# Kernel tuning notes

Measured on AMD Instinct MI355X. Metric: run time of the kernel, lower is better.

The kernel has to match this reference:

```python
import jax, jax.numpy as jnp
import numpy as np

# Irreps config: input/output = 32x0e + 16x1o (dim 80), H=4 heads -> head = 8x0e + 4x1o (dim 20)
M0, M1 = 32, 16      # input muls for 0e / 1o
m0, m1 = 8, 4        # per-head muls
H = 4
HEAD_DIM = m0 + 3 * m1   # 20
WNUM = H * (M0 * m0 + M1 * m0 + M0 * m1 + M1 * m1)  # 2304 per-edge TP weights
NB, HID = 16, 64
SQRT3 = np.float32(np.sqrt(3.0))
EPS = 1e-8


def radial_mlp(x, W1, b1, W2, b2):
    return jax.nn.silu(x @ W1 + b1) @ W2 + b2


def tp_edge(ss, vv, sh0, sh1, w):
    """FullyConnectedTensorProduct (32x0e+16x1o) x (1x0e+1x1o) -> H*(8x0e+4x1o) with per-edge weights w [E, WNUM].
    Paths: 0e*0e->0e, 1o*1o->0e (CG dot/sqrt3), 0e*1o->1o, 1o*0e->1o; path norm 1/sqrt(fan_in)."""
    E = ss.shape[0]
    per = M0 * m0 + M1 * m0 + M0 * m1 + M1 * m1  # 576
    w = w.reshape(E, H, per)
    o = 0
    Wss = w[..., o:o + M0 * m0].reshape(E, H, M0, m0); o += M0 * m0
    Wvv = w[..., o:o + M1 * m0].reshape(E, H, M1, m0); o += M1 * m0
    Wsv = w[..., o:o + M0 * m1].reshape(E, H, M0, m1); o += M0 * m1
    Wvs = w[..., o:o + M1 * m1].reshape(E, H, M1, m1)
    fan = np.float32(np.sqrt(M0 + M1))  # fan_in = 48 for both output irreps
    vv_dot = jnp.einsum('eui,ei->eu', vv, sh1) / SQRT3
    out0 = (jnp.einsum('eu,ehuw->ehw', ss * sh0[:, None], Wss)
            + jnp.einsum('eu,ehuw->ehw', vv_dot, Wvv)) / fan          # [E,H,m0]
    out1 = (jnp.einsum('eu,ehuw->ehw', ss, Wsv)[..., None] * sh1[:, None, None, :]
            + jnp.einsum('eui,ehuw->ehwi', vv * sh0[:, None, None], Wvs)) / fan  # [E,H,m1,3]
    return out0, out1


def setup_inputs() -> dict:
    key = jax.random.key(0)
    ks = jax.random.split(key, 24)
    N, E = 2000, 32000
    g = lambda k, s, sc=1.0: jax.random.normal(k, s, jnp.float32) * sc
    inp = {}
    inp['node_features'] = g(ks[0], (N, M0 + 3 * M1))
    inp['edge_index'] = jax.random.randint(ks[1], (2, E), 0, N)
    inp['edge_sh'] = g(ks[2], (E, 4))
    inp['edge_radial_emb'] = jax.random.uniform(ks[3], (E, NB), jnp.float32)
    # query e3nn Linear (per-head blocks)
    inp['Wq0'] = g(ks[4], (H, M0, m0))
    inp['Wq1'] = g(ks[5], (H, M1, m1))
    # radial MLPs for key / value TP weights
    inp['Wk1'] = g(ks[6], (NB, HID), 1 / np.sqrt(NB)); inp['bk1'] = jnp.zeros((HID,), jnp.float32)
    inp['Wk2'] = g(ks[7], (HID, WNUM), 1 / np.sqrt(HID)); inp['bk2'] = jnp.zeros((WNUM,), jnp.float32)
    inp['Wv1'] = g(ks[8], (NB, HID), 1 / np.sqrt(NB)); inp['bv1'] = jnp.zeros((HID,), jnp.float32)
    inp['Wv2'] = g(ks[9], (HID, WNUM), 1 / np.sqrt(HID)); inp['bv2'] = jnp.zeros((WNUM,), jnp.float32)
    # single-head dot-product TP -> 0e (shared weights)
    inp['Wd0'] = g(ks[10], (m0, m0))
    inp['Wd1'] = g(ks[11], (m1, m1))
    # output projection Linear (all heads mixed per irrep)
    inp['Wo0'] = g(ks[12], (H * m0, M0))
    inp['Wo1'] = g(ks[13], (H * m1, M1))
    # FFN: out irreps -> (2*M0)x0e + M1x1o -> out irreps
    inp['Wf1_0'] = g(ks[14], (M0, 2 * M0))
    inp['Wf1_1'] = g(ks[15], (M1, M1))
    inp['Wf2_0'] = g(ks[16], (2 * M0, M0))
    inp['Wf2_1'] = g(ks[17], (M1, M1))
    return inp


def reference(node_features, edge_index, edge_sh, edge_radial_emb,
              Wq0, Wq1, Wk1, bk1, Wk2, bk2, Wv1, bv1, Wv2, bv2,
              Wd0, Wd1, Wo0, Wo1, Wf1_0, Wf1_1, Wf2_0, Wf2_1):
    N = node_features.shape[0]
    s = node_features[:, :M0]                       # [N, M0] scalars
    v = node_features[:, M0:].reshape(N, M1, 3)     # [N, M1, 3] vectors
    src, dst = edge_index[0], edge_index[1]

    # query Linear (e3nn: per-irrep channel mix, norm 1/sqrt(fan_in))
    q0 = jnp.einsum('nu,huw->nhw', s, Wq0) / np.sqrt(M0)
    q1 = jnp.einsum('nui,huw->nhwi', v, Wq1) / np.sqrt(M1)

    sh0, sh1 = edge_sh[:, 0], edge_sh[:, 1:4]
    ss, vv = s[src], v[src]                         # gather per edge

    wk = radial_mlp(edge_radial_emb, Wk1, bk1, Wk2, bk2)
    wv = radial_mlp(edge_radial_emb, Wv1, bv1, Wv2, bv2)
    k0, k1 = tp_edge(ss, vv, sh0, sh1, wk)
    v0, v1 = tp_edge(ss, vv, sh0, sh1, wv)

    # per-head equivariant dot product -> 0e logits
    qd0, qd1 = q0[dst], q1[dst]
    fan_d = np.float32(np.sqrt(m0 * m0 + m1 * m1))
    logits = (jnp.einsum('ehu,uv,ehv->eh', qd0, Wd0, k0)
              + jnp.einsum('ehui,uv,ehvi->eh', qd1, Wd1, k1) / SQRT3) / fan_d
    logits = logits / np.sqrt(HEAD_DIM)             # self.scale
    logits = jnp.clip(logits, -10.0, 10.0)

    # scatter softmax over edges sharing a destination node
    seg_max = jax.ops.segment_max(logits, dst, num_segments=N)
    seg_max = jnp.maximum(seg_max, -10.0)           # handle empty segments
    ex = jnp.exp(logits - seg_max[dst])
    denom = jax.ops.segment_sum(ex, dst, num_segments=N)
    alpha = ex / (denom[dst] + 1e-12)               # [E, H]

    agg0 = jax.ops.segment_sum(alpha[..., None] * v0, dst, num_segments=N)        # [N,H,m0]
    agg1 = jax.ops.segment_sum(alpha[..., None, None] * v1, dst, num_segments=N)  # [N,H,m1,3]

    # output projection Linear over concatenated heads
    o0 = agg0.reshape(N, H * m0) @ Wo0 / np.sqrt(H * m0)
    o1 = jnp.einsum('nui,uw->nwi', agg1.reshape(N, H * m1, 3), Wo1) / np.sqrt(H * m1)

    # residual (input irreps == output irreps -> identity skip)
    x0 = s + o0
    x1 = v + o1

    # FFN with SafeNormActivation
    f0 = x0 @ Wf1_0 / np.sqrt(M0)                               # [N, 2*M0]
    f1 = jnp.einsum('nui,uw->nwi', x1, Wf1_1) / np.sqrt(M1)     # [N, M1, 3]
    a0 = jax.nn.silu(f0)
    norms = jnp.linalg.norm(f1, axis=-1, keepdims=True)
    safe = jnp.maximum(norms, EPS)
    a1 = jnp.where(norms < EPS, 0.0, (f1 / safe) * jax.nn.silu(norms))
    g0 = a0 @ Wf2_0 / np.sqrt(2 * M0)
    g1 = jnp.einsum('nui,uw->nwi', a1, Wf2_1) / np.sqrt(M1)

    out0 = x0 + g0
    out1 = x1 + g1
    return jnp.concatenate([out0, out1.reshape(N, M1 * 3)], axis=-1)
```

## Files before the change

### kernel.cpp

```cpp
#include <hip/hip_runtime.h>

typedef unsigned int uint;
typedef unsigned short ushort;
typedef __attribute__((ext_vector_type(8))) short bf16x8;
typedef __attribute__((ext_vector_type(4))) float f32x4;

#define N_NODES 2000
#define N_EDGES 32000
#define WNUM 2304

constexpr size_t OFF_AGG0 = 0;
constexpr size_t OFF_AGG1 = 64000;
constexpr size_t OFF_DEN  = 160000;
constexpr size_t OFF_CNT  = 168000;
constexpr size_t OFF_FLAG = 170000;
constexpr size_t OFF_W2T  = 170004;
constexpr size_t OFF_QT0  = 317460;
constexpr size_t OFF_QT1  = 381460;
constexpr size_t OFF_EORD = 477460;

__device__ __forceinline__ float b2f(ushort u){ union{uint i; float f;}x; x.i=((uint)u)<<16; return x.f; }
__device__ __forceinline__ float lo16(uint w){ union{uint u; float f;}x; x.u=w<<16; return x.f; }
__device__ __forceinline__ float hi16(uint w){ union{uint u; float f;}x; x.u=w&0xFFFF0000u; return x.f; }
__device__ __forceinline__ ushort f2b(float f){
  union{float f; uint u;}x; x.f=f;
  uint r = (x.u + 0x7FFFu + ((x.u>>16)&1u)) >> 16;
  return (ushort)r;
}
__device__ __forceinline__ float siluf(float x){ return x / (1.f + __expf(-x)); }

template<bool F32>
__device__ __forceinline__ float ldf(const void* p, int i){
  if (F32) return ((const float*)p)[i];
  return b2f(((const ushort*)p)[i]);
}
__device__ __forceinline__ float ldfr(const void* p, int i, bool f32){
  return f32 ? ((const float*)p)[i] : b2f(((const ushort*)p)[i]);
}

template<bool F32>
__device__ void prep_body(
    const void* __restrict__ nf, const int* __restrict__ eidx,
    const void* __restrict__ Wk2, const void* __restrict__ Wv2,
    const void* __restrict__ Wq0, const void* __restrict__ Wq1,
    const void* __restrict__ Wd0, const void* __restrict__ Wd1,
    ushort* __restrict__ W2T, float* __restrict__ qt0, float* __restrict__ qt1,
    int* __restrict__ cnt){
  const int t = threadIdx.x;
  const int bid = blockIdx.x;

  if (bid < 72){
    __shared__ ushort tile[64][66];
    const int mat = bid / 36, jt = bid - mat*36;
    const void* W = mat ? Wv2 : Wk2;
    const int j0 = jt*64;
    const int jo = t & 63, cb = t >> 6;
    #pragma unroll
    for (int k=0; k<16; ++k){
      const int c = cb + k*4;
      tile[c][jo] = F32 ? f2b(((const float*)W)[(size_t)c*WNUM + j0 + jo])
                        : ((const ushort*)W)[(size_t)c*WNUM + j0 + jo];
    }
    __syncthreads();
    const int jl = t >> 2, c0 = (t & 3)*16;
    ushort* dst = W2T + (size_t)mat*147456 + (size_t)(j0+jl)*64 + c0;
    #pragma unroll
    for (int k=0; k<16; ++k) dst[k] = tile[c0+k][jl];
  } else if (bid < 104){
    __shared__ float nfL[64][80];
    __shared__ float wq0L[1024], wq1L[256], wd0L[64], wd1L[16];
    const int nb = bid - 72, n0 = nb*64;
    for (int idx=t; idx<64*80; idx+=256){
      const int nn = n0 + idx/80;
      nfL[idx/80][idx%80] = (nn < N_NODES) ? ldf<F32>(nf, nn*80 + idx%80) : 0.f;
    }
    for (int idx=t; idx<1024; idx+=256) wq0L[idx] = ldf<F32>(Wq0, idx);
    if (t < 256) wq1L[t] = ldf<F32>(Wq1, t);
    if (t < 64)  wd0L[t] = ldf<F32>(Wd0, t);
    if (t < 16)  wd1L[t] = ldf<F32>(Wd1, t);
    __syncthreads();
    const int nl = t >> 2, h = t & 3;
    const int nn = n0 + nl;
    if (nn < N_NODES){
      const float* S = &nfL[nl][0];
      float q0[8];
      #pragma unroll
      for (int w=0; w<8; ++w){
        float a = 0.f;
        #pragma unroll
        for (int u=0; u<32; ++u) a += S[u]*wq0L[h*256 + u*8 + w];
        q0[w] = a * 0.17677669529663687f;
      }
      #pragma unroll
      for (int vv=0; vv<8; ++vv){
        float a = 0.f;
        #pragma unroll
        for (int u=0; u<8; ++u) a += q0[u]*wd0L[u*8+vv];
        qt0[nn*32 + h*8 + vv] = a;
      }
      float q1[12];
      #pragma unroll
      for (int w=0; w<4; ++w)
        #pragma unroll
        for (int i=0; i<3; ++i){
          float a = 0.f;
          #pragma unroll
          for (int u=0; u<16; ++u) a += S[32+u*3+i]*wq1L[h*64 + u*4 + w];
          q1[w*3+i] = a * 0.25f;
        }
      #pragma unroll
      for (int vv=0; vv<4; ++vv)
        #pragma unroll
        for (int i=0; i<3; ++i){
          float a = 0.f;
          #pragma unroll
          for (int u=0; u<4; ++u) a += q1[u*3+i]*wd1L[u*4+vv];
          qt1[nn*48 + h*12 + vv*3 + i] = a;
        }
    }
  } else {
    const int e = (bid-104)*256 + t;
    if (e < N_EDGES) atomicAdd(cnt + eidx[N_EDGES + e], 1);
  }
}

__global__ __launch_bounds__(256) void prep_kernel(
    const void* nf, const int* eidx,
    const void* Wk2, const void* Wv2,
    const void* Wq0, const void* Wq1,
    const void* Wd0, const void* Wd1,
    ushort* W2T, float* qt0, float* qt1,
    int* cnt, int* flag){
  __shared__ int s_cnt;
  const int t = threadIdx.x;
  if (t == 0) s_cnt = 0;
  __syncthreads();
  {
    uint u = ((const ushort*)nf)[t*2];
    uint ex = (u >> 7) & 0xFFu;
    if (ex >= 0xA0u) atomicAdd(&s_cnt, 1);
  }
  __syncthreads();
  const bool F32 = (s_cnt >= 20);
  if (blockIdx.x == 0 && t == 0) *flag = F32 ? 1 : 0;
  if (F32) prep_body<true >(nf, eidx, Wk2, Wv2, Wq0, Wq1, Wd0, Wd1, W2T, qt0, qt1, cnt);
  else     prep_body<false>(nf, eidx, Wk2, Wv2, Wq0, Wq1, Wd0, Wd1, W2T, qt0, qt1, cnt);
}

__global__ __launch_bounds__(256) void scan_kernel(int* __restrict__ cnt){
  __shared__ int ls[256];
  const int t = threadIdx.x;
  const int base = t*8;
  int v[8]; int s = 0;
  #pragma unroll
  for (int k=0; k<8; ++k){ int idx = base+k; v[k] = (idx < N_NODES) ? cnt[idx] : 0; s += v[k]; }
  ls[t] = s; __syncthreads();
  for (int off=1; off<256; off<<=1){
    int x = (t >= off) ? ls[t-off] : 0;
    __syncthreads();
    ls[t] += x;
    __syncthreads();
  }
  int ex = ls[t] - s;
  #pragma unroll
  for (int k=0; k<8; ++k){ int idx = base+k; if (idx < N_NODES){ int c = v[k]; cnt[idx] = ex; ex += c; } }
}

__global__ __launch_bounds__(256) void scat_kernel(const int* __restrict__ eidx,
                                                   int* __restrict__ cnt, int* __restrict__ eord){
  int e = blockIdx.x*256 + threadIdx.x;
  if (e < N_EDGES){
    int p = atomicAdd(cnt + eidx[N_EDGES + e], 1);
    eord[p] = e;
  }
}

struct Smem {
  ushort hidA[2][32][72];
  union {
    struct {
      float fssT[32][36];
      float fvvT[16][36];
      float sslT[32][36];
    } f;
    float cont[4][32][21];
  } u;
  float vshT[16][3][36];
  float sh1T[3][36];
  int   dstL[32];
};

template<bool F32>
__device__ void edge_body(
    const void* __restrict__ nf,  const int* __restrict__ eidx,
    const int* __restrict__ eord,
    const void* __restrict__ esh, const void* __restrict__ emb,
    const void* __restrict__ Wk1, const void* __restrict__ bk1, const void* __restrict__ bk2,
    const void* __restrict__ Wv1, const void* __restrict__ bv1, const void* __restrict__ bv2,
    const ushort* __restrict__ W2T,
    const float* __restrict__ qt0g, const float* __restrict__ qt1g,
    float* __restrict__ agg0, float* __restrict__ agg1, float* __restrict__ denom,
    Smem& sm){
  const int t  = threadIdx.x;
  const int hw = t >> 5;
  const int r  = t & 31;
  const int geb = blockIdx.x*32;

  #pragma unroll 1
  for (int e=0; e<4; ++e){
    const int le = hw*4+e;
    const int ge = eord[geb+le];
    const int src = eidx[ge], d = eidx[N_EDGES+ge];
    const float sh0 = ldf<F32>(esh, ge*4+0);
    const float s1a = ldf<F32>(esh, ge*4+1), s1b = ldf<F32>(esh, ge*4+2), s1c = ldf<F32>(esh, ge*4+3);
    if (r == 0) sm.dstL[le] = d;
    if (r < 3) sm.sh1T[r][le] = (r==0)? s1a : (r==1)? s1b : s1c;
    float sv = ldf<F32>(nf, src*80 + r);
    sm.u.f.sslT[r][le] = sv;
    sm.u.f.fssT[r][le] = sv * sh0;
    if (r < 16){
      float v0 = ldf<F32>(nf, src*80+32+r*3+0);
      float v1 = ldf<F32>(nf, src*80+32+r*3+1);
      float v2 = ldf<F32>(nf, src*80+32+r*3+2);
      sm.vshT[r][0][le] = v0*sh0; sm.vshT[r][1][le] = v1*sh0; sm.vshT[r][2][le] = v2*sh0;
      sm.u.f.fvvT[r][le] = (v0*s1a + v1*s1b + v2*s1c) * 0.5773502691896258f;
    }
  }

  #pragma unroll 1
  for (int e=0; e<4; ++e){
    const int le = hw*4+e;
    const int ge = eord[geb+le];
    float em[16];
    if (F32){
      const float4* p = (const float4*)((const float*)emb + ge*16);
      float4 a=p[0], b=p[1], c=p[2], d4=p[3];
      em[0]=a.x; em[1]=a.y; em[2]=a.z; em[3]=a.w;
      em[4]=b.x; em[5]=b.y; em[6]=b.z; em[7]=b.w;
      em[8]=c.x; em[9]=c.y; em[10]=c.z; em[11]=c.w;
      em[12]=d4.x; em[13]=d4.y; em[14]=d4.z; em[15]=d4.w;
    } else {
      const uint4* p = (const uint4*)((const ushort*)emb + ge*16);
      uint4 a=p[0], b=p[1];
      em[0]=lo16(a.x); em[1]=hi16(a.x); em[2]=lo16(a.y); em[3]=hi16(a.y);
      em[4]=lo16(a.z); em[5]=hi16(a.z); em[6]=lo16(a.w); em[7]=hi16(a.w);
      em[8]=lo16(b.x); em[9]=hi16(b.x); em[10]=lo16(b.y); em[11]=hi16(b.y);
      em[12]=lo16(b.z); em[13]=hi16(b.z); em[14]=lo16(b.w); em[15]=hi16(b.w);
    }
    #pragma unroll
    for (int cc=0; cc<2; ++cc){
      const int c = r + cc*32;
      float ak = ldf<F32>(bk1, c), av = ldf<F32>(bv1, c);
      #pragma unroll
      for (int b=0; b<16; ++b){
        ak += em[b] * ldf<F32>(Wk1, b*64 + c);
        av += em[b] * ldf<F32>(Wv1, b*64 + c);
      }
      sm.hidA[0][le][c] = f2b(siluf(ak));
      sm.hidA[1][le][c] = f2b(siluf(av));
    }
  }
  __syncthreads();

  const int h = t >> 6;
  const int lane = t & 63, q = lane >> 4, n = lane & 15;
  const float invfan = 0.14433756729740643f;
  float exv[2][4];

  #pragma unroll 1
  for (int kv=0; kv<2; ++kv){
    const ushort* wmat = W2T + (size_t)kv*147456;
    const void* bvec = kv ? bv2 : bk2;
    bf16x8 af[2][2];
    #pragma unroll
    for (int Mt=0; Mt<2; ++Mt)
      #pragma unroll
      for (int kh=0; kh<2; ++kh)
        af[Mt][kh] = *(const bf16x8*)&sm.hidA[kv][Mt*16+n][kh*32 + q*8];

    float a0[2][4], aP[2][4], aW[3][2][4];
    #pragma unroll
    for (int Mt=0; Mt<2; ++Mt)
      #pragma unroll
      for (int z=0; z<4; ++z){
        a0[Mt][z]=0.f; aP[Mt][z]=0.f;
        aW[0][Mt][z]=0.f; aW[1][Mt][z]=0.f; aW[2][Mt][z]=0.f;
      }

    #pragma unroll 4
    for (int tl=0; tl<24; ++tl){
      const size_t tb = ((size_t)((h*36+tl)*16 + n))*64 + q*8;
      bf16x8 b0 = *(const bf16x8*)(wmat + tb), b1 = *(const bf16x8*)(wmat + tb + 32);
      const float bb = ldf<F32>(bvec, h*576 + tl*16 + n);
      const bool ss = (tl < 16);
      const int u = ss ? (tl*2 + (n>>3)) : ((tl-16)*2 + (n>>3));
      #pragma unroll
      for (int Mt=0; Mt<2; ++Mt){
        f32x4 fv = ss ? *(const f32x4*)&sm.u.f.fssT[u][Mt*16+q*4]
                      : *(const f32x4*)&sm.u.f.fvvT[u][Mt*16+q*4];
        f32x4 c = {bb,bb,bb,bb};
        c = __builtin_amdgcn_mfma_f32_16x16x32_bf16(af[Mt][0], b0, c, 0,0,0);
        c = __builtin_amdgcn_mfma_f32_16x16x32_bf16(af[Mt][1], b1, c, 0,0,0);
        #pragma unroll
        for (int z=0; z<4; ++z) a0[Mt][z] += c[z]*fv[z];
      }
    }
    #pragma unroll 4
    for (int tl=24; tl<32; ++tl){
      const size_t tb = ((size_t)((h*36+tl)*16 + n))*64 + q*8;
      bf16x8 b0 = *(const bf16x8*)(wmat + tb), b1 = *(const bf16x8*)(wmat + tb + 32);
      const float bb = ldf<F32>(bvec, h*576 + tl*16 + n);
      const int u = (tl-24)*4 + (n>>2);
      #pragma unroll
      for (int Mt=0; Mt<2; ++Mt){
        f32x4 fv = *(const f32x4*)&sm.u.f.sslT[u][Mt*16+q*4];
        f32x4 c = {bb,bb,bb,bb};
        c = __builtin_amdgcn_mfma_f32_16x16x32_bf16(af[Mt][0], b0, c, 0,0,0);
        c = __builtin_amdgcn_mfma_f32_16x16x32_bf16(af[Mt][1], b1, c, 0,0,0);
        #pragma unroll
        for (int z=0; z<4; ++z) aP[Mt][z] += c[z]*fv[z];
      }
    }
    #pragma unroll
    for (int tl=32; tl<36; ++tl){
      const size_t tb = ((size_t)((h*36+tl)*16 + n))*64 + q*8;
      bf16x8 b0 = *(const bf16x8*)(wmat + tb), b1 = *(const bf16x8*)(wmat + tb + 32);
      const float bb = ldf<F32>(bvec, h*576 + tl*16 + n);
      const int u = (tl-32)*4 + (n>>2);
      #pragma unroll
      for (int Mt=0; Mt<2; ++Mt){
        f32x4 c = {bb,bb,bb,bb};
        c = __builtin_amdgcn_mfma_f32_16x16x32_bf16(af[Mt][0], b0, c, 0,0,0);
        c = __builtin_amdgcn_mfma_f32_16x16x32_bf16(af[Mt][1], b1, c, 0,0,0);
        #pragma unroll
        for (int i=0; i<3; ++i){
          f32x4 fv = *(const f32x4*)&sm.vshT[u][i][Mt*16+q*4];
          #pragma unroll
          for (int z=0; z<4; ++z) aW[i][Mt][z] += c[z]*fv[z];
        }
      }
    }

    #pragma unroll
    for (int Mt=0; Mt<2; ++Mt)
      #pragma unroll
      for (int z=0; z<4; ++z){
        a0[Mt][z] += __shfl_xor(a0[Mt][z], 8, 64);
        aP[Mt][z] += __shfl_xor(aP[Mt][z], 4, 64);
        aP[Mt][z] += __shfl_xor(aP[Mt][z], 8, 64);
        #pragma unroll
        for (int i=0; i<3; ++i){
          aW[i][Mt][z] += __shfl_xor(aW[i][Mt][z], 4, 64);
          aW[i][Mt][z] += __shfl_xor(aW[i][Mt][z], 8, 64);
        }
      }

    if (kv == 0){
      float lgp[2][4];
      #pragma unroll
      for (int Mt=0; Mt<2; ++Mt)
        #pragma unroll
        for (int z=0; z<4; ++z){
          const int el = Mt*16 + q*4 + z;
          const int d = sm.dstL[el];
          float acc = 0.f;
          if (n < 8) acc = qt0g[d*32 + h*8 + n] * a0[Mt][z];
          if (n < 4){
            float s = 0.f;
            #pragma unroll
            for (int i=0; i<3; ++i){
              float k1 = aP[Mt][z]*sm.sh1T[i][el] + aW[i][Mt][z];
              s += qt1g[d*48 + h*12 + n*3 + i] * k1;
            }
            acc += s * 0.5773502691896258f;
          }
          lgp[Mt][z] = acc;
        }
      #pragma unroll
      for (int Mt=0; Mt<2; ++Mt)
        #pragma unroll
        for (int z=0; z<4; ++z){
          lgp[Mt][z] += __shfl_xor(lgp[Mt][z], 1, 64);
          lgp[Mt][z] += __shfl_xor(lgp[Mt][z], 2, 64);
          lgp[Mt][z] += __shfl_xor(lgp[Mt][z], 4, 64);
          lgp[Mt][z] += __shfl_xor(lgp[Mt][z], 8, 64);
          float lg = lgp[Mt][z] * invfan * 0.025f;
          lg = fminf(10.f, fmaxf(-10.f, lg));
          exv[Mt][z] = __expf(lg - 10.0f);
        }
    } else {
      __syncthreads();
      #pragma unroll
      for (int Mt=0; Mt<2; ++Mt)
        #pragma unroll
        for (int z=0; z<4; ++z){
          const int el = Mt*16 + q*4 + z;
          const float ex = exv[Mt][z];
          if (n == 0) sm.u.cont[h][el][0] = ex;
          if (n < 8)  sm.u.cont[h][el][1+n] = ex * a0[Mt][z] * invfan;
          if (n < 4){
            #pragma unroll
            for (int i=0; i<3; ++i){
              float v1 = (aP[Mt][z]*sm.sh1T[i][el] + aW[i][Mt][z]) * invfan;
              sm.u.cont[h][el][9+n*3+i] = ex * v1;
            }
          }
        }
    }
  }
  __syncthreads();

  if (t < 84){
    const int h2 = t / 21, comp = t - h2*21;
    float acc = 0.f;
    #pragma unroll 1
    for (int e2=0; e2<32; ++e2){
      acc += sm.u.cont[h2][e2][comp];
      const int d2 = sm.dstL[e2];
      if (e2 == 31 || sm.dstL[e2+1] != d2){
        if (comp == 0)      atomicAdd(denom + d2*4  + h2, acc);
        else if (comp < 9)  atomicAdd(agg0  + d2*32 + h2*8  + (comp-1), acc);
        else                atomicAdd(agg1  + d2*48 + h2*12 + (comp-9), acc);
        acc = 0.f;
      }
    }
  }
}

__global__ __launch_bounds__(256) void edge_kernel(
    const void* nf, const int* eidx, const int* eord, const void* esh, const void* emb,
    const void* Wk1, const void* bk1, const void* bk2,
    const void* Wv1, const void* bv1, const void* bv2,
    const ushort* W2T, const float* qt0g, const float* qt1g,
    float* agg0, float* agg1, float* denom, const int* flag){
  __shared__ Smem sm;
  if (*flag)
    edge_body<true >(nf,eidx,eord,esh,emb,Wk1,bk1,bk2,Wv1,bv1,bv2,W2T,qt0g,qt1g,agg0,agg1,denom,sm);
  else
    edge_body<false>(nf,eidx,eord,esh,emb,Wk1,bk1,bk2,Wv1,bv1,bv2,W2T,qt0g,qt1g,agg0,agg1,denom,sm);
}

__global__ __launch_bounds__(64) void node_out_kernel(
    const void* __restrict__ nf, const float* __restrict__ agg0r, const float* __restrict__ agg1r,
    const float* __restrict__ denom,
    const void* __restrict__ Wo0, const void* __restrict__ Wo1,
    const void* __restrict__ Wf10, const void* __restrict__ Wf11,
    const void* __restrict__ Wf20, const void* __restrict__ Wf21,
    void* __restrict__ out, const int* __restrict__ flag){
  __shared__ float ag0[32], ag1[48], adiv[4];
  __shared__ float x0s[32], x1s[48], a0s[64], f1s[48], coefs[16];
  const bool F32 = (*flag) != 0;
  const int n = blockIdx.x, t = threadIdx.x;
  if (t < 4) adiv[t] = 1.f / (denom[n*4+t] + 1e-12f);
  __syncthreads();
  if (t < 32) ag0[t] = agg0r[n*32+t] * adiv[t>>3];
  if (t < 48) ag1[t] = agg1r[n*48+t] * adiv[t/12];
  __syncthreads();
  if (t < 32){
    float o = 0.f;
    #pragma unroll
    for (int k=0; k<32; ++k) o += ag0[k]*ldfr(Wo0, k*32+t, F32);
    x0s[t] = ldfr(nf, n*80+t, F32) + o*0.17677669529663687f;
  }
  if (t < 48){
    int w = t/3, i = t - w*3;
    float o = 0.f;
    #pragma unroll
    for (int u=0; u<16; ++u) o += ag1[u*3+i]*ldfr(Wo1, u*16+w, F32);
    x1s[t] = ldfr(nf, n*80+32+t, F32) + o*0.25f;
  }
  __syncthreads();
  {
    float f0 = 0.f;
    #pragma unroll
    for (int u=0; u<32; ++u) f0 += x0s[u]*ldfr(Wf10, u*64+t, F32);
    a0s[t] = siluf(f0*0.17677669529663687f);
  }
  if (t < 48){
    int w = t/3, i = t - w*3;
    float f1 = 0.f;
    #pragma unroll
    for (int u=0; u<16; ++u) f1 += x1s[u*3+i]*ldfr(Wf11, u*16+w, F32);
    f1s[t] = f1*0.25f;
  }
  __syncthreads();
  if (t < 16){
    float a = f1s[t*3], b = f1s[t*3+1], c = f1s[t*3+2];
    float nrm = sqrtf(a*a+b*b+c*c);
    float safe = fmaxf(nrm, 1e-8f);
    coefs[t] = (nrm < 1e-8f) ? 0.f : siluf(nrm)/safe;
  }
  __syncthreads();
  if (t < 32){
    float g = 0.f;
    #pragma unroll
    for (int u=0; u<64; ++u) g += a0s[u]*ldfr(Wf20, u*32+t, F32);
    float val = x0s[t] + g*0.125f;
    if (F32) ((float*)out)[n*80+t] = val; else ((ushort*)out)[n*80+t] = f2b(val);
  }
  if (t < 48){
    int w = t/3, i = t - w*3;
    float g = 0.f;
    #pragma unroll
    for (int u=0; u<16; ++u) g += coefs[u]*f1s[u*3+i]*ldfr(Wf21, u*16+w, F32);
    float val = x1s[t] + g*0.25f;
    if (F32) ((float*)out)[n*80+32+t] = val; else ((ushort*)out)[n*80+32+t] = f2b(val);
  }
}

extern "C" void kernel_launch(void* const* d_in, const int* in_sizes, int n_in,
                              void* d_out, int out_size, void* d_ws, size_t ws_size,
                              hipStream_t stream){
  const void* nf   = d_in[0];
  const int*  eidx = (const int*)d_in[1];
  const void* esh  = d_in[2];
  const void* emb  = d_in[3];
  const void* Wq0  = d_in[4];
  const void* Wq1  = d_in[5];
  const void* Wk1  = d_in[6];
  const void* bk1  = d_in[7];
  const void* Wk2  = d_in[8];
  const void* bk2  = d_in[9];
  const void* Wv1  = d_in[10];
  const void* bv1  = d_in[11];
  const void* Wv2  = d_in[12];
  const void* bv2  = d_in[13];
  const void* Wd0  = d_in[14];
  const void* Wd1  = d_in[15];
  const void* Wo0  = d_in[16];
  const void* Wo1  = d_in[17];
  const void* Wf10 = d_in[18];
  const void* Wf11 = d_in[19];
  const void* Wf20 = d_in[20];
  const void* Wf21 = d_in[21];
  float* ws = (float*)d_ws;

  float* agg0  = ws + OFF_AGG0;
  float* agg1  = ws + OFF_AGG1;
  float* denom = ws + OFF_DEN;
  int*   cnt   = (int*)(ws + OFF_CNT);
  int*   flag  = (int*)(ws + OFF_FLAG);
  ushort* W2T  = (ushort*)(ws + OFF_W2T);
  float* qt0   = ws + OFF_QT0;
  float* qt1   = ws + OFF_QT1;
  int*   eord  = (int*)(ws + OFF_EORD);

  hipMemsetAsync(agg0, 0, 170000*sizeof(float), stream);
  prep_kernel<<<229, 256, 0, stream>>>(nf, eidx, Wk2, Wv2, Wq0, Wq1, Wd0, Wd1,
                                       W2T, qt0, qt1, cnt, flag);
  scan_kernel<<<1, 256, 0, stream>>>(cnt);
  scat_kernel<<<125, 256, 0, stream>>>(eidx, cnt, eord);
  edge_kernel<<<N_EDGES/32, 256, 0, stream>>>(nf, eidx, eord, esh, emb,
                                              Wk1, bk1, bk2, Wv1, bv1, bv2,
                                              W2T, qt0, qt1,
                                              agg0, agg1, denom, flag);
  node_out_kernel<<<N_NODES, 64, 0, stream>>>(nf, agg0, agg1, denom,
                                              Wo0, Wo1, Wf10, Wf11, Wf20, Wf21, d_out, flag);
}
```

Baseline: 236.4 us.

## Process 64 edges per block to reuse weight fragments across more MFMA tiles

Doubles the edges handled per workgroup from 32 to 64, so each loaded W2T B-fragment feeds four M-tiles instead of two. The goal is to halve global weight traffic per edge. Shared-memory arrays are resized, vshT moves into the union, and the softmax exponents go through shared memory instead of registers to offset the extra register pressure. Risks are higher register use and LDS footprint lowering occupancy, and only 500 blocks for the grid.

Measured after the change: 250.8 us. 1.06x slower.

```diff
diff --git a/kernel.cpp b/kernel.cpp
--- a/kernel.cpp
+++ b/kernel.cpp
@@ -8,6 +8,7 @@
 #define N_NODES 2000
 #define N_EDGES 32000
 #define WNUM 2304
+#define EPB 64
 
 constexpr size_t OFF_AGG0 = 0;
 constexpr size_t OFF_AGG1 = 64000;
@@ -176,18 +177,19 @@
 }
 
 struct Smem {
-  ushort hidA[2][32][72];
+  ushort hidA[2][64][72];
   union {
     struct {
-      float fssT[32][36];
-      float fvvT[16][36];
-      float sslT[32][36];
+      float fssT[32][66];
+      float fvvT[16][66];
+      float sslT[32][66];
+      float vshT[16][3][66];
     } f;
-    float cont[4][32][21];
+    float cont[4][64][21];
   } u;
-  float vshT[16][3][36];
-  float sh1T[3][36];
-  int   dstL[32];
+  float sh1T[3][66];
+  float exL[4][64];
+  int   dstL[64];
 };
 
 template<bool F32>
@@ -204,11 +206,11 @@
   const int t  = threadIdx.x;
   const int hw = t >> 5;
   const int r  = t & 31;
-  const int geb = blockIdx.x*32;
+  const int geb = blockIdx.x*EPB;
 
   #pragma unroll 1
-  for (int e=0; e<4; ++e){
-    const int le = hw*4+e;
+  for (int e=0; e<8; ++e){
+    const int le = hw*8+e;
     const int ge = eord[geb+le];
     const int src = eidx[ge], d = eidx[N_EDGES+ge];
     const float sh0 = ldf<F32>(esh, ge*4+0);
@@ -222,14 +224,14 @@
       float v0 = ldf<F32>(nf, src*80+32+r*3+0);
       float v1 = ldf<F32>(nf, src*80+32+r*3+1);
       float v2 = ldf<F32>(nf, src*80+32+r*3+2);
-      sm.vshT[r][0][le] = v0*sh0; sm.vshT[r][1][le] = v1*sh0; sm.vshT[r][2][le] = v2*sh0;
+      sm.u.f.vshT[r][0][le] = v0*sh0; sm.u.f.vshT[r][1][le] = v1*sh0; sm.u.f.vshT[r][2][le] = v2*sh0;
       sm.u.f.fvvT[r][le] = (v0*s1a + v1*s1b + v2*s1c) * 0.5773502691896258f;
     }
   }
 
   #pragma unroll 1
-  for (int e=0; e<4; ++e){
-    const int le = hw*4+e;
+  for (int e=0; e<8; ++e){
+    const int le = hw*8+e;
     const int ge = eord[geb+le];
     float em[16];
     if (F32){
@@ -265,29 +267,28 @@
   const int h = t >> 6;
   const int lane = t & 63, q = lane >> 4, n = lane & 15;
   const float invfan = 0.14433756729740643f;
-  float exv[2][4];
 
   #pragma unroll 1
   for (int kv=0; kv<2; ++kv){
     const ushort* wmat = W2T + (size_t)kv*147456;
     const void* bvec = kv ? bv2 : bk2;
-    bf16x8 af[2][2];
-    #pragma unroll
-    for (int Mt=0; Mt<2; ++Mt)
+    bf16x8 af[4][2];
+    #pragma unroll
+    for (int Mt=0; Mt<4; ++Mt)
       #pragma unroll
       for (int kh=0; kh<2; ++kh)
         af[Mt][kh] = *(const bf16x8*)&sm.hidA[kv][Mt*16+n][kh*32 + q*8];
 
-    float a0[2][4], aP[2][4], aW[3][2][4];
-    #pragma unroll
-    for (int Mt=0; Mt<2; ++Mt)
+    float a0[4][4], aP[4][4], aW[3][4][4];
+    #pragma unroll
+    for (int Mt=0; Mt<4; ++Mt)
       #pragma unroll
       for (int z=0; z<4; ++z){
         a0[Mt][z]=0.f; aP[Mt][z]=0.f;
         aW[0][Mt][z]=0.f; aW[1][Mt][z]=0.f; aW[2][Mt][z]=0.f;
       }
 
-    #pragma unroll 4
+    #pragma unroll 2
     for (int tl=0; tl<24; ++tl){
       const size_t tb = ((size_t)((h*36+tl)*16 + n))*64 + q*8;
       bf16x8 b0 = *(const bf16x8*)(wmat + tb), b1 = *(const bf16x8*)(wmat + tb + 32);
@@ -295,7 +296,7 @@
       const bool ss = (tl < 16);
       const int u = ss ? (tl*2 + (n>>3)) : ((tl-16)*2 + (n>>3));
       #pragma unroll
-      for (int Mt=0; Mt<2; ++Mt){
+      for (int Mt=0; Mt<4; ++Mt){
         f32x4 fv = ss ? *(const f32x4*)&sm.u.f.fssT[u][Mt*16+q*4]
                       : *(const f32x4*)&sm.u.f.fvvT[u][Mt*16+q*4];
         f32x4 c = {bb,bb,bb,bb};
@@ -305,14 +306,14 @@
         for (int z=0; z<4; ++z) a0[Mt][z] += c[z]*fv[z];
       }
     }
-    #pragma unroll 4
+    #pragma unroll 2
     for (int tl=24; tl<32; ++tl){
       const size_t tb = ((size_t)((h*36+tl)*16 + n))*64 + q*8;
       bf16x8 b0 = *(const bf16x8*)(wmat + tb), b1 = *(const bf16x8*)(wmat + tb + 32);
       const float bb = ldf<F32>(bvec, h*576 + tl*16 + n);
       const int u = (tl-24)*4 + (n>>2);
       #pragma unroll
-      for (int Mt=0; Mt<2; ++Mt){
+      for (int Mt=0; Mt<4; ++Mt){
         f32x4 fv = *(const f32x4*)&sm.u.f.sslT[u][Mt*16+q*4];
         f32x4 c = {bb,bb,bb,bb};
         c = __builtin_amdgcn_mfma_f32_16x16x32_bf16(af[Mt][0], b0, c, 0,0,0);
@@ -328,13 +329,13 @@
       const float bb = ldf<F32>(bvec, h*576 + tl*16 + n);
       const int u = (tl-32)*4 + (n>>2);
       #pragma unroll
-      for (int Mt=0; Mt<2; ++Mt){
+      for (int Mt=0; Mt<4; ++Mt){
         f32x4 c = {bb,bb,bb,bb};
         c = __builtin_amdgcn_mfma_f32_16x16x32_bf16(af[Mt][0], b0, c, 0,0,0);
         c = __builtin_amdgcn_mfma_f32_16x16x32_bf16(af[Mt][1], b1, c, 0,0,0);
         #pragma unroll
         for (int i=0; i<3; ++i){
-          f32x4 fv = *(const f32x4*)&sm.vshT[u][i][Mt*16+q*4];
+          f32x4 fv = *(const f32x4*)&sm.u.f.vshT[u][i][Mt*16+q*4];
           #pragma unroll
           for (int z=0; z<4; ++z) aW[i][Mt][z] += c[z]*fv[z];
         }
@@ -342,7 +343,7 @@
     }
 
     #pragma unroll
-    for (int Mt=0; Mt<2; ++Mt)
+    for (int Mt=0; Mt<4; ++Mt)
       #pragma unroll
       for (int z=0; z<4; ++z){
         a0[Mt][z] += __shfl_xor(a0[Mt][z], 8, 64);
@@ -356,9 +357,8 @@
       }
 
     if (kv == 0){
-      float lgp[2][4];
-      #pragma unroll
-      for (int Mt=0; Mt<2; ++Mt)
+      #pragma unroll
+      for (int Mt=0; Mt<4; ++Mt)
         #pragma unroll
         for (int z=0; z<4; ++z){
           const int el = Mt*16 + q*4 + z;
@@ -374,28 +374,22 @@
             }
             acc += s * 0.5773502691896258f;
           }
-          lgp[Mt][z] = acc;
-        }
-      #pragma unroll
-      for (int Mt=0; Mt<2; ++Mt)
-        #pragma unroll
-        for (int z=0; z<4; ++z){
-          lgp[Mt][z] += __shfl_xor(lgp[Mt][z], 1, 64);
-          lgp[Mt][z] += __shfl_xor(lgp[Mt][z], 2, 64);
-          lgp[Mt][z] += __shfl_xor(lgp[Mt][z], 4, 64);
-          lgp[Mt][z] += __shfl_xor(lgp[Mt][z], 8, 64);
-          float lg = lgp[Mt][z] * invfan * 0.025f;
+          acc += __shfl_xor(acc, 1, 64);
+          acc += __shfl_xor(acc, 2, 64);
+          acc += __shfl_xor(acc, 4, 64);
+          acc += __shfl_xor(acc, 8, 64);
+          float lg = acc * invfan * 0.025f;
           lg = fminf(10.f, fmaxf(-10.f, lg));
-          exv[Mt][z] = __expf(lg - 10.0f);
+          if (n == 0) sm.exL[h][el] = __expf(lg - 10.0f);
         }
     } else {
       __syncthreads();
       #pragma unroll
-      for (int Mt=0; Mt<2; ++Mt)
+      for (int Mt=0; Mt<4; ++Mt)
         #pragma unroll
         for (int z=0; z<4; ++z){
           const int el = Mt*16 + q*4 + z;
-          const float ex = exv[Mt][z];
+          const float ex = sm.exL[h][el];
           if (n == 0) sm.u.cont[h][el][0] = ex;
           if (n < 8)  sm.u.cont[h][el][1+n] = ex * a0[Mt][z] * invfan;
           if (n < 4){
@@ -414,10 +408,10 @@
     const int h2 = t / 21, comp = t - h2*21;
     float acc = 0.f;
     #pragma unroll 1
-    for (int e2=0; e2<32; ++e2){
+    for (int e2=0; e2<EPB; ++e2){
       acc += sm.u.cont[h2][e2][comp];
       const int d2 = sm.dstL[e2];
-      if (e2 == 31 || sm.dstL[e2+1] != d2){
+      if (e2 == EPB-1 || sm.dstL[e2+1] != d2){
         if (comp == 0)      atomicAdd(denom + d2*4  + h2, acc);
         else if (comp < 9)  atomicAdd(agg0  + d2*32 + h2*8  + (comp-1), acc);
         else                atomicAdd(agg1  + d2*48 + h2*12 + (comp-9), acc);
@@ -550,10 +544,10 @@
                                        W2T, qt0, qt1, cnt, flag);
   scan_kernel<<<1, 256, 0, stream>>>(cnt);
   scat_kernel<<<125, 256, 0, stream>>>(eidx, cnt, eord);
-  edge_kernel<<<N_EDGES/32, 256, 0, stream>>>(nf, eidx, eord, esh, emb,
-                                              Wk1, bk1, bk2, Wv1, bv1, bv2,
-                                              W2T, qt0, qt1,
-                                              agg0, agg1, denom, flag);
+  edge_kernel<<<N_EDGES/EPB, 256, 0, stream>>>(nf, eidx, eord, esh, emb,
+                                               Wk1, bk1, bk2, Wv1, bv1, bv2,
+                                               W2T, qt0, qt1,
+                                               agg0, agg1, denom, flag);
   node_out_kernel<<<N_NODES, 64, 0, stream>>>(nf, agg0, agg1, denom,
                                               Wo0, Wo1, Wf10, Wf11, Wf20, Wf21, d_out, flag);
 }
```
